# Kernel optimization log

Measured on AMD Instinct MI355X. Metric: run time of the kernel, lower is better.

The kernel has to match this reference:

```python
import jax, jax.numpy as jnp
import numpy as np

C_M = 256
C_Z = 128
S = 256   # number of MSA sequences (global `s` in source)
R = 384   # number of residues (global `r` in source)
C = 32    # per-head channel dim
H = 8     # N_head
EPS = 1e-5


def _layer_norm(x, w, b):
    mu = jnp.mean(x, axis=-1, keepdims=True)
    var = jnp.mean(jnp.square(x - mu), axis=-1, keepdims=True)
    return (x - mu) * jax.lax.rsqrt(var + EPS) * w + b


def setup_inputs() -> dict:
    key = jax.random.key(0)
    ks = jax.random.split(key, 8)
    w = 0.02
    return {
        "msa": jax.random.normal(ks[0], (S, R, C_M), dtype=jnp.float32),
        "pair": jax.random.normal(ks[1], (R, R, C_Z), dtype=jnp.float32),
        "norm_msa_w": jnp.ones((H, C_M), jnp.float32),
        "norm_msa_b": jnp.zeros((H, C_M), jnp.float32),
        "wq": jax.random.normal(ks[2], (H, C, C_M), dtype=jnp.float32) * w,
        "wk": jax.random.normal(ks[3], (H, C, C_M), dtype=jnp.float32) * w,
        "wv": jax.random.normal(ks[4], (H, C, C_M), dtype=jnp.float32) * w,
        "norm_pair_w": jnp.ones((H, C_Z), jnp.float32),
        "norm_pair_b": jnp.zeros((H, C_Z), jnp.float32),
        "wb": jax.random.normal(ks[5], (H, S, C_Z), dtype=jnp.float32) * w,
        "wg": jax.random.normal(ks[6], (H, C, C_M), dtype=jnp.float32) * w,
        "out_w": jax.random.normal(ks[7], (C_M, C * H), dtype=jnp.float32) * w,
        "out_b": jnp.zeros((C_M,), jnp.float32),
    }


def reference(msa, pair, norm_msa_w, norm_msa_b, wq, wk, wv,
              norm_pair_w, norm_pair_b, wb, wg, out_w, out_b):
    inv_sqrt_c = 1.0 / np.sqrt(C).astype(np.float32)
    pair_flat = pair.reshape(-1, C_Z)  # (R*R, C_Z); view(-1, c_z)
    outs = []
    for i in range(H):
        # NOTE: faithful to source — msa is OVERWRITTEN by the per-head norm,
        # so normalization compounds across the head loop.
        msa = _layer_norm(msa, norm_msa_w[i], norm_msa_b[i])
        q = jnp.einsum('src,dc->srd', msa, wq[i])  # (S,R,C)
        k = jnp.einsum('src,dc->srd', msa, wk[i])
        v = jnp.einsum('src,dc->srd', msa, wv[i])
        # pair bias: LN -> Linear(c_z -> s) -> reshape (not transpose!) to (S,R,R)
        b = jnp.einsum('pc,sc->ps', _layer_norm(pair_flat, norm_pair_w[i], norm_pair_b[i]), wb[i])
        b = b.reshape(S, R, R)
        g = jax.nn.sigmoid(jnp.einsum('src,dc->srd', msa, wg[i]))  # (S,R,C)
        logits = inv_sqrt_c * (jnp.einsum('src,stc->srt', q, k) + b)  # (S,R,R)
        a = jax.nn.softmax(logits, axis=-2)  # softmax over QUERY axis, as in source
        o = g * jnp.einsum('srt,stc->src', a, v)  # (S,R,C)
        outs.append(o)
    out = jnp.concatenate(outs, axis=2)  # (S,R,C*H)
    return jnp.einsum('srk,mk->srm', out, out_w) + out_b  # (S,R,C_M)
```

## Files before the change

kernel.cpp:

```cpp
#include <hip/hip_runtime.h>

typedef unsigned short bf16_t;
typedef uint4  __attribute__((may_alias)) uint4_a;
typedef uint2  __attribute__((may_alias)) uint2_a;
typedef float4 __attribute__((may_alias)) float4_a;
typedef short bf16x8 __attribute__((ext_vector_type(8)));
typedef bf16x8 __attribute__((may_alias)) bf16x8_a;
typedef float f32x4 __attribute__((ext_vector_type(4)));

#define MFMA16(a, b, c) __builtin_amdgcn_mfma_f32_16x16x32_bf16((a), (b), (c), 0, 0, 0)

constexpr int kS  = 256;
constexpr int kR  = 384;
constexpr int kCM = 256;
constexpr int kCZ = 128;
constexpr int kC  = 32;
constexpr int kH  = 8;
constexpr int kP  = kR * kR;
constexpr int kM  = kS * kR;

#define EPSF 1e-5f
#define SCALEF 0.17677669529663687f

__device__ __forceinline__ float bf2f(bf16_t u) {
  return __uint_as_float(((unsigned int)u) << 16);
}
__device__ __forceinline__ bf16_t f2bf(float f) {
  unsigned int u = __float_as_uint(f);
  u += 0x7fffu + ((u >> 16) & 1u);
  return (bf16_t)(u >> 16);
}

__global__ __launch_bounds__(256) void k_pair_fused(const float* __restrict__ pair,
                                                    bf16_t* __restrict__ pair_bf,
                                                    float* __restrict__ mu,
                                                    float* __restrict__ rstd) {
  int row = blockIdx.x * 8 + (threadIdx.x >> 5);
  int l = threadIdx.x & 31;
  const float* src = pair + (size_t)row * kCZ + l * 4;
  float4_a x = *(const float4_a*)src;
  float s1 = x.x + x.y + x.z + x.w;
  float s2 = x.x * x.x + x.y * x.y + x.z * x.z + x.w * x.w;
#pragma unroll
  for (int off = 16; off > 0; off >>= 1) {
    s1 += __shfl_xor(s1, off);
    s2 += __shfl_xor(s2, off);
  }
  float m = s1 * (1.0f / kCZ);
  float v = s2 * (1.0f / kCZ) - m * m;
  float rs = rsqrtf(fmaxf(v, 0.0f) + EPSF);
  if (l == 0) {
    mu[row] = m;
    rstd[row] = rs;
  }
  uint2 u;
  u.x = (unsigned)f2bf(x.x) | ((unsigned)f2bf(x.y) << 16);
  u.y = (unsigned)f2bf(x.z) | ((unsigned)f2bf(x.w) << 16);
  *(uint2_a*)(pair_bf + (size_t)row * kCZ + l * 4) = u;
}

__global__ __launch_bounds__(256) void k_msa_ln(const float* __restrict__ src_f,
                                                const bf16_t* __restrict__ src_b,
                                                bf16_t* __restrict__ dst,
                                                const float* __restrict__ wall,
                                                const float* __restrict__ ball,
                                                int head, int first) {
  int row = blockIdx.x * 8 + (threadIdx.x >> 5);
  int l = threadIdx.x & 31;
  int c0 = l * 8;
  float x[8];
  if (first) {
    float4_a a = *(const float4_a*)(src_f + (size_t)row * kCM + c0);
    float4_a b = *(const float4_a*)(src_f + (size_t)row * kCM + c0 + 4);
    x[0] = a.x; x[1] = a.y; x[2] = a.z; x[3] = a.w;
    x[4] = b.x; x[5] = b.y; x[6] = b.z; x[7] = b.w;
  } else {
    union { bf16x8 v; bf16_t h[8]; } uu;
    uu.v = *(const bf16x8_a*)(src_b + (size_t)row * kCM + c0);
#pragma unroll
    for (int j = 0; j < 8; ++j) x[j] = bf2f(uu.h[j]);
  }
  float s1 = 0.f, s2 = 0.f;
#pragma unroll
  for (int j = 0; j < 8; ++j) {
    s1 += x[j];
    s2 += x[j] * x[j];
  }
#pragma unroll
  for (int off = 16; off > 0; off >>= 1) {
    s1 += __shfl_xor(s1, off);
    s2 += __shfl_xor(s2, off);
  }
  float m = s1 * (1.0f / kCM);
  float var = s2 * (1.0f / kCM) - m * m;
  float rs = rsqrtf(fmaxf(var, 0.0f) + EPSF);
  float4_a wa = *(const float4_a*)(wall + head * kCM + c0);
  float4_a wb4 = *(const float4_a*)(wall + head * kCM + c0 + 4);
  float4_a ba = *(const float4_a*)(ball + head * kCM + c0);
  float4_a bb4 = *(const float4_a*)(ball + head * kCM + c0 + 4);
  float wv[8] = {wa.x, wa.y, wa.z, wa.w, wb4.x, wb4.y, wb4.z, wb4.w};
  float bv[8] = {ba.x, ba.y, ba.z, ba.w, bb4.x, bb4.y, bb4.z, bb4.w};
  bf16_t h[8];
#pragma unroll
  for (int j = 0; j < 8; ++j) h[j] = f2bf((x[j] - m) * rs * wv[j] + bv[j]);
  uint4 u;
  u.x = (unsigned)h[0] | ((unsigned)h[1] << 16);
  u.y = (unsigned)h[2] | ((unsigned)h[3] << 16);
  u.z = (unsigned)h[4] | ((unsigned)h[5] << 16);
  u.w = (unsigned)h[6] | ((unsigned)h[7] << 16);
  *(uint4_a*)(dst + (size_t)row * kCM + c0) = u;
}

__global__ __launch_bounds__(256) void k_pack_wcat_all(const float* __restrict__ wq,
                                                       const float* __restrict__ wk,
                                                       const float* __restrict__ wv,
                                                       const float* __restrict__ wg,
                                                       bf16_t* __restrict__ Wcat) {
  int gid = blockIdx.x * 256 + threadIdx.x;
  int head = gid >> 15;
  int idx = gid & 32767;
  int j = idx >> 8;
  int c = idx & 255;
  const float* src = (j < 32) ? wq : (j < 64) ? wk : (j < 96) ? wv : wg;
  int d = j & 31;
  Wcat[gid] = f2bf(src[(head * kC + d) * kCM + c]);
}

__global__ __launch_bounds__(256) void k_pack_bias_all(const float* __restrict__ wb,
                                                       const float* __restrict__ npw,
                                                       const float* __restrict__ npb,
                                                       bf16_t* __restrict__ wbeff,
                                                       float* __restrict__ beta,
                                                       float* __restrict__ sw) {
  int head = blockIdx.x;
  int j = threadIdx.x;
  float sb = 0.f, ssw = 0.f;
  for (int c = 0; c < kCZ; ++c) {
    float w = wb[(head * kS + j) * kCZ + c];
    float e = w * npw[head * kCZ + c] * SCALEF;
    wbeff[(size_t)head * kS * kCZ + j * kCZ + c] = f2bf(e);
    ssw += e;
    sb += w * npb[head * kCZ + c];
  }
  sw[head * kS + j] = ssw;
  beta[head * kS + j] = sb * SCALEF;
}

__global__ __launch_bounds__(256) void k_pack_outw(const float* __restrict__ in,
                                                   bf16_t* __restrict__ out) {
  int i = blockIdx.x * 256 + threadIdx.x;
  out[i] = f2bf(in[i]);
}

__global__ __launch_bounds__(256) void k_gemm_qkvg_mx(const bf16_t* __restrict__ A,
                                                      const bf16_t* __restrict__ B,
                                                      bf16_t* __restrict__ q,
                                                      bf16_t* __restrict__ k,
                                                      bf16_t* __restrict__ v,
                                                      bf16_t* __restrict__ g_all,
                                                      int head) {
  __shared__ bf16_t As[128 * 32];
  __shared__ bf16_t Bs[128 * 32];
  int m0 = blockIdx.x * 128;
  int tid = threadIdx.x;
  int w = tid >> 6, L = tid & 63, l15 = L & 15, q4 = L >> 4;
  int wm = w >> 1, wn = w & 1;
  f32x4 acc[4][4] = {};
  for (int k0 = 0; k0 < 256; k0 += 32) {
#pragma unroll
    for (int rep = 0; rep < 2; ++rep) {
      int idx = tid + rep * 256;
      int row = idx >> 2, sg = idx & 3;
      *(uint4_a*)&As[row * 32 + sg * 8] = *(const uint4_a*)(A + (size_t)(m0 + row) * 256 + k0 + sg * 8);
      *(uint4_a*)&Bs[row * 32 + sg * 8] = *(const uint4_a*)(B + (size_t)row * 256 + k0 + sg * 8);
    }
    __syncthreads();
    bf16x8 af[4], bfr[4];
#pragma unroll
    for (int mt = 0; mt < 4; ++mt) af[mt] = *(const bf16x8_a*)&As[(wm * 64 + mt * 16 + l15) * 32 + q4 * 8];
#pragma unroll
    for (int nt = 0; nt < 4; ++nt) bfr[nt] = *(const bf16x8_a*)&Bs[(wn * 64 + nt * 16 + l15) * 32 + q4 * 8];
#pragma unroll
    for (int mt = 0; mt < 4; ++mt)
#pragma unroll
      for (int nt = 0; nt < 4; ++nt) acc[mt][nt] = MFMA16(af[mt], bfr[nt], acc[mt][nt]);
    __syncthreads();
  }
#pragma unroll
  for (int mt = 0; mt < 4; ++mt)
#pragma unroll
    for (int nt = 0; nt < 4; ++nt) {
      int n = wn * 64 + nt * 16 + l15;
      int mat = n >> 5, d = n & 31;
#pragma unroll
      for (int i = 0; i < 4; ++i) {
        int m = m0 + wm * 64 + mt * 16 + q4 * 4 + i;
        float val = acc[mt][nt][i];
        if (mat == 0) {
          q[(size_t)m * kC + d] = f2bf(val * SCALEF);
        } else if (mat == 1) {
          k[(size_t)m * kC + d] = f2bf(val);
        } else if (mat == 2) {
          v[(size_t)m * kC + d] = f2bf(val);
        } else {
          float sg = 1.0f / (1.0f + __expf(-val));
          g_all[(size_t)m * kCM + head * kC + d] = f2bf(sg);
        }
      }
    }
}

__global__ __launch_bounds__(256) void k_gemm_bias_mx(const bf16_t* __restrict__ A,
                                                      const bf16_t* __restrict__ B,
                                                      const float* __restrict__ mu,
                                                      const float* __restrict__ rstd,
                                                      const float* __restrict__ sw,
                                                      const float* __restrict__ beta,
                                                      bf16_t* __restrict__ Bm) {
  __shared__ bf16_t As[128 * 32];
  __shared__ bf16_t Bs[128 * 32];
  int m0 = blockIdx.x * 128;
  int n0 = blockIdx.y * 128;
  int tid = threadIdx.x;
  int w = tid >> 6, L = tid & 63, l15 = L & 15, q4 = L >> 4;
  int wm = w >> 1, wn = w & 1;
  f32x4 acc[4][4] = {};
  for (int k0 = 0; k0 < 128; k0 += 32) {
#pragma unroll
    for (int rep = 0; rep < 2; ++rep) {
      int idx = tid + rep * 256;
      int row = idx >> 2, sg = idx & 3;
      *(uint4_a*)&As[row * 32 + sg * 8] = *(const uint4_a*)(A + (size_t)(m0 + row) * 128 + k0 + sg * 8);
      *(uint4_a*)&Bs[row * 32 + sg * 8] = *(const uint4_a*)(B + (size_t)(n0 + row) * 128 + k0 + sg * 8);
    }
    __syncthreads();
    bf16x8 af[4], bfr[4];
#pragma unroll
    for (int mt = 0; mt < 4; ++mt) af[mt] = *(const bf16x8_a*)&As[(wm * 64 + mt * 16 + l15) * 32 + q4 * 8];
#pragma unroll
    for (int nt = 0; nt < 4; ++nt) bfr[nt] = *(const bf16x8_a*)&Bs[(wn * 64 + nt * 16 + l15) * 32 + q4 * 8];
#pragma unroll
    for (int mt = 0; mt < 4; ++mt)
#pragma unroll
      for (int nt = 0; nt < 4; ++nt) acc[mt][nt] = MFMA16(af[mt], bfr[nt], acc[mt][nt]);
    __syncthreads();
  }
#pragma unroll
  for (int mt = 0; mt < 4; ++mt)
#pragma unroll
    for (int i = 0; i < 4; ++i) {
      int m = m0 + wm * 64 + mt * 16 + q4 * 4 + i;
      float mp = mu[m], rp = rstd[m];
#pragma unroll
      for (int nt = 0; nt < 4; ++nt) {
        int n = n0 + wn * 64 + nt * 16 + l15;
        float val = rp * (acc[mt][nt][i] - mp * sw[n]) + beta[n];
        Bm[(size_t)m * kS + n] = f2bf(val);
      }
    }
}

__global__ __launch_bounds__(256, 1) void k_attn(const bf16_t* __restrict__ q,
                                                 const bf16_t* __restrict__ kmat,
                                                 const bf16_t* __restrict__ v,
                                                 const bf16_t* __restrict__ Bm,
                                                 float* __restrict__ o0,
                                                 float* __restrict__ o1,
                                                 int head) {
  int tb = blockIdx.x;
  int s  = blockIdx.y;
  int tid = threadIdx.x;
  int w = tid >> 6, L = tid & 63, l15 = L & 15, q4 = L >> 4;
  float* opart = tb ? o1 : o0;
  __shared__ bf16_t vT[32 * 200];
  __shared__ bf16_t Psh[64 * 192];

  int tbase = tb * 192;
#pragma unroll
  for (int rep = 0; rep < 3; ++rep) {
    int idx = tid + rep * 256;
    int t = idx >> 2, sg = idx & 3;
    union { uint4 u; bf16_t h[8]; } uu;
    uu.u = *(const uint4_a*)(v + (size_t)(s * kR + tbase + t) * kC + sg * 8);
#pragma unroll
    for (int j = 0; j < 8; ++j) vT[(sg * 8 + j) * 200 + t] = uu.h[j];
  }
  __syncthreads();
  bf16x8 bfv[12];
#pragma unroll
  for (int kk = 0; kk < 6; ++kk)
#pragma unroll
    for (int ct = 0; ct < 2; ++ct)
      bfv[kk * 2 + ct] = *(const bf16x8_a*)&vT[(ct * 16 + l15) * 200 + kk * 32 + q4 * 8];

  int t0 = tbase + 48 * w;
  const bf16_t* bmS = Bm + (size_t)s * kP;
  f32x4 acc[24][3];
#pragma unroll
  for (int rt = 0; rt < 24; ++rt)
#pragma unroll
    for (int tt = 0; tt < 3; ++tt)
#pragma unroll
      for (int i = 0; i < 4; ++i)
        acc[rt][tt][i] = bf2f(bmS[(size_t)(rt * 16 + q4 * 4 + i) * kR + t0 + tt * 16 + l15]);

  const bf16_t* qs = q + (size_t)s * kR * kC;
  const bf16_t* kp = kmat + (size_t)s * kR * kC;
  bf16x8 bk[3];
#pragma unroll
  for (int tt = 0; tt < 3; ++tt)
    bk[tt] = *(const bf16x8_a*)(kp + (size_t)(t0 + tt * 16 + l15) * kC + q4 * 8);
#pragma unroll
  for (int rt = 0; rt < 24; ++rt) {
    bf16x8 af = *(const bf16x8_a*)(qs + (size_t)(rt * 16 + l15) * kC + q4 * 8);
#pragma unroll
    for (int tt = 0; tt < 3; ++tt) acc[rt][tt] = MFMA16(af, bk[tt], acc[rt][tt]);
  }

  float mx[3] = {-3.0e38f, -3.0e38f, -3.0e38f};
#pragma unroll
  for (int rt = 0; rt < 24; ++rt)
#pragma unroll
    for (int tt = 0; tt < 3; ++tt)
#pragma unroll
      for (int i = 0; i < 4; ++i) mx[tt] = fmaxf(mx[tt], acc[rt][tt][i]);
#pragma unroll
  for (int tt = 0; tt < 3; ++tt) {
    mx[tt] = fmaxf(mx[tt], __shfl_xor(mx[tt], 16));
    mx[tt] = fmaxf(mx[tt], __shfl_xor(mx[tt], 32));
  }
  float sm[3] = {0.f, 0.f, 0.f};
#pragma unroll
  for (int rt = 0; rt < 24; ++rt)
#pragma unroll
    for (int tt = 0; tt < 3; ++tt)
#pragma unroll
      for (int i = 0; i < 4; ++i) {
        float e = __expf(acc[rt][tt][i] - mx[tt]);
        acc[rt][tt][i] = e;
        sm[tt] += e;
      }
#pragma unroll
  for (int tt = 0; tt < 3; ++tt) {
    sm[tt] += __shfl_xor(sm[tt], 16);
    sm[tt] += __shfl_xor(sm[tt], 32);
  }
  float di[3];
#pragma unroll
  for (int tt = 0; tt < 3; ++tt) di[tt] = 1.0f / sm[tt];

#pragma unroll
  for (int c = 0; c < 6; ++c) {
#pragma unroll
    for (int j = 0; j < 4; ++j)
#pragma unroll
      for (int tt = 0; tt < 3; ++tt)
#pragma unroll
        for (int i = 0; i < 4; ++i) {
          int rl = j * 16 + q4 * 4 + i;
          int tl = 48 * w + tt * 16 + l15;
          Psh[rl * 192 + (tl ^ ((rl & 7) << 3))] = f2bf(acc[4 * c + j][tt][i] * di[tt]);
        }
    __syncthreads();
    f32x4 pacc[2] = {};
    int rr = w * 16 + l15;
#pragma unroll
    for (int kk = 0; kk < 6; ++kk) {
      int e = kk * 32 + q4 * 8;
      bf16x8 af = *(const bf16x8_a*)&Psh[rr * 192 + (e ^ ((rr & 7) << 3))];
#pragma unroll
      for (int ct = 0; ct < 2; ++ct) pacc[ct] = MFMA16(af, bfv[kk * 2 + ct], pacc[ct]);
    }
#pragma unroll
    for (int ct = 0; ct < 2; ++ct)
#pragma unroll
      for (int i = 0; i < 4; ++i) {
        int r = c * 64 + w * 16 + q4 * 4 + i;
        int cc = ct * 16 + l15;
        opart[(size_t)(s * kR + r) * kCM + head * kC + cc] = pacc[ct][i];
      }
    __syncthreads();
  }
}

__global__ __launch_bounds__(256) void k_gemm_final_mx(const float* __restrict__ pA,
                                                       const float* __restrict__ pB,
                                                       const bf16_t* __restrict__ gall,
                                                       const bf16_t* __restrict__ Bw,
                                                       const float* __restrict__ bias,
                                                       float* __restrict__ out) {
  __shared__ bf16_t As[2 * 64 * 32];
  __shared__ bf16_t Bs[256 * 32];
  int m0 = blockIdx.x * 64;
  int tid = threadIdx.x;
  int w = tid >> 6, L = tid & 63, l15 = L & 15, q4 = L >> 4;
  f32x4 acc[4][4] = {};
  for (int kc = 0; kc < 256; kc += 32) {
    {
      int row = tid >> 2, sg = tid & 3;
      size_t base = (size_t)(m0 + row) * kCM + kc + sg * 8;
      float4_a a0 = *(const float4_a*)(pA + base);
      float4_a a1 = *(const float4_a*)(pA + base + 4);
      float4_a b0 = *(const float4_a*)(pB + base);
      float4_a b1 = *(const float4_a*)(pB + base + 4);
      union { bf16x8 v; bf16_t h[8]; } gg;
      gg.v = *(const bf16x8_a*)(gall + base);
      float ff[8] = {a0.x + b0.x, a0.y + b0.y, a0.z + b0.z, a0.w + b0.w,
                     a1.x + b1.x, a1.y + b1.y, a1.z + b1.z, a1.w + b1.w};
#pragma unroll
      for (int j = 0; j < 8; ++j) ff[j] *= bf2f(gg.h[j]);
      uint4 uh, ul;
      bf16_t hi[8], lo[8];
#pragma unroll
      for (int j = 0; j < 8; ++j) {
        hi[j] = f2bf(ff[j]);
        lo[j] = f2bf(ff[j] - bf2f(hi[j]));
      }
      uh.x = (unsigned)hi[0] | ((unsigned)hi[1] << 16); uh.y = (unsigned)hi[2] | ((unsigned)hi[3] << 16);
      uh.z = (unsigned)hi[4] | ((unsigned)hi[5] << 16); uh.w = (unsigned)hi[6] | ((unsigned)hi[7] << 16);
      ul.x = (unsigned)lo[0] | ((unsigned)lo[1] << 16); ul.y = (unsigned)lo[2] | ((unsigned)lo[3] << 16);
      ul.z = (unsigned)lo[4] | ((unsigned)lo[5] << 16); ul.w = (unsigned)lo[6] | ((unsigned)lo[7] << 16);
      *(uint4_a*)&As[row * 32 + sg * 8] = uh;
      *(uint4_a*)&As[2048 + row * 32 + sg * 8] = ul;
    }
#pragma unroll
    for (int rep = 0; rep < 4; ++rep) {
      int idx = tid + rep * 256;
      int row = idx >> 2, sg = idx & 3;
      *(uint4_a*)&Bs[row * 32 + sg * 8] = *(const uint4_a*)(Bw + (size_t)row * kCM + kc + sg * 8);
    }
    __syncthreads();
    bf16x8 bfr[4];
#pragma unroll
    for (int nt = 0; nt < 4; ++nt) bfr[nt] = *(const bf16x8_a*)&Bs[(w * 64 + nt * 16 + l15) * 32 + q4 * 8];
#pragma unroll
    for (int half = 0; half < 2; ++half)
#pragma unroll
      for (int mt = 0; mt < 4; ++mt) {
        bf16x8 af = *(const bf16x8_a*)&As[half * 2048 + (mt * 16 + l15) * 32 + q4 * 8];
#pragma unroll
        for (int nt = 0; nt < 4; ++nt) acc[mt][nt] = MFMA16(af, bfr[nt], acc[mt][nt]);
      }
    __syncthreads();
  }
#pragma unroll
  for (int mt = 0; mt < 4; ++mt)
#pragma unroll
    for (int nt = 0; nt < 4; ++nt) {
      int n = w * 64 + nt * 16 + l15;
      float bn = bias[n];
#pragma unroll
      for (int i = 0; i < 4; ++i) {
        int m = m0 + mt * 16 + q4 * 4 + i;
        out[(size_t)m * kCM + n] = acc[mt][nt][i] + bn;
      }
    }
}

extern "C" void kernel_launch(void* const* d_in, const int* in_sizes, int n_in,
                              void* d_out, int out_size, void* d_ws, size_t ws_size,
                              hipStream_t stream) {
  (void)in_sizes; (void)n_in; (void)out_size; (void)ws_size;
  const float* msa_in = (const float*)d_in[0];
  const float* pair   = (const float*)d_in[1];
  const float* nmw    = (const float*)d_in[2];
  const float* nmb    = (const float*)d_in[3];
  const float* wq     = (const float*)d_in[4];
  const float* wk     = (const float*)d_in[5];
  const float* wv     = (const float*)d_in[6];
  const float* npw    = (const float*)d_in[7];
  const float* npb    = (const float*)d_in[8];
  const float* wb     = (const float*)d_in[9];
  const float* wg     = (const float*)d_in[10];
  const float* outw   = (const float*)d_in[11];
  const float* outb   = (const float*)d_in[12];
  float* out = (float*)d_out;

  char* ws = (char*)d_ws;
  size_t off = 0;
  bf16_t* msa_cur  = (bf16_t*)(ws + off); off += (size_t)kM * kCM * 2;
  bf16_t* pair_bf  = (bf16_t*)(ws + off); off += (size_t)kP * kCZ * 2;
  bf16_t* Bm       = (bf16_t*)(ws + off); off += (size_t)kP * kS * 2;
  bf16_t* qb       = (bf16_t*)(ws + off); off += (size_t)kM * kC * 2;
  bf16_t* kb       = (bf16_t*)(ws + off); off += (size_t)kM * kC * 2;
  bf16_t* vb       = (bf16_t*)(ws + off); off += (size_t)kM * kC * 2;
  bf16_t* g_all    = (bf16_t*)(ws + off); off += (size_t)kM * kCM * 2;
  float*  pB       = (float*)(ws + off);  off += (size_t)kM * kCM * 4;
  float* mu_p      = (float*)(ws + off);  off += (size_t)kP * 4;
  float* rstd_p    = (float*)(ws + off);  off += (size_t)kP * 4;
  bf16_t* Wcat_all = (bf16_t*)(ws + off); off += (size_t)kH * 128 * 256 * 2;
  bf16_t* wbef_all = (bf16_t*)(ws + off); off += (size_t)kH * 256 * 128 * 2;
  bf16_t* outw_bf  = (bf16_t*)(ws + off); off += (size_t)256 * 256 * 2;
  float* beta_all  = (float*)(ws + off);  off += (size_t)kH * 256 * 4;
  float* sw_all    = (float*)(ws + off);  off += (size_t)kH * 256 * 4;

  k_pair_fused<<<kP / 8, 256, 0, stream>>>(pair, pair_bf, mu_p, rstd_p);
  k_pack_outw<<<256, 256, 0, stream>>>(outw, outw_bf);
  k_pack_wcat_all<<<kH * 128, 256, 0, stream>>>(wq, wk, wv, wg, Wcat_all);
  k_pack_bias_all<<<kH, 256, 0, stream>>>(wb, npw, npb, wbef_all, beta_all, sw_all);

  for (int h = 0; h < kH; ++h) {
    k_msa_ln<<<kM / 8, 256, 0, stream>>>(msa_in, msa_cur, msa_cur, nmw, nmb, h, h == 0 ? 1 : 0);
    k_gemm_qkvg_mx<<<kM / 128, 256, 0, stream>>>(msa_cur, Wcat_all + (size_t)h * 128 * 256,
                                                 qb, kb, vb, g_all, h);
    k_gemm_bias_mx<<<dim3(kP / 128, 2), 256, 0, stream>>>(pair_bf, wbef_all + (size_t)h * 256 * 128,
                                                          mu_p, rstd_p,
                                                          sw_all + h * 256, beta_all + h * 256, Bm);
    k_attn<<<dim3(2, kS), 256, 0, stream>>>(qb, kb, vb, Bm, out, pB, h);
  }

  k_gemm_final_mx<<<kM / 64, 256, 0, stream>>>(out, pB, g_all, outw_bf, outb, out);
}
```

Baseline: 1.325 ms.

## Fuse pair-bias GEMM into attention kernel and emit gated bf16 hi/lo output

Removes the separate pair-bias GEMM that wrote a large bf16 bias tensor (R*R*S) to global memory each head. Each attention block now computes its sequence's bias slice on the fly from pair_bf and the bias weights into LDS, then loads it into the logits accumulators. The two key-halves are handled in one block, which drops the split fp32 partial outputs. Gating and the hi/lo bf16 split move into the attention epilogue, so the final GEMM just loads bf16. The trade-off is half as many blocks (256), heavy LDS use and more serialized work per block. That could reduce occupancy and overlap.

```diff
diff --git a/kernel.cpp b/kernel.cpp
--- a/kernel.cpp
+++ b/kernel.cpp
@@ -21,6 +21,7 @@
 
 #define EPSF 1e-5f
 #define SCALEF 0.17677669529663687f
+#define BSWZ(i) ((i) ^ ((((i) >> 8) & 7) << 4))
 
 __device__ __forceinline__ float bf2f(bf16_t u) {
   return __uint_as_float(((unsigned int)u) << 16);
@@ -210,182 +211,224 @@
     }
 }
 
-__global__ __launch_bounds__(256) void k_gemm_bias_mx(const bf16_t* __restrict__ A,
-                                                      const bf16_t* __restrict__ B,
-                                                      const float* __restrict__ mu,
-                                                      const float* __restrict__ rstd,
-                                                      const float* __restrict__ sw,
-                                                      const float* __restrict__ beta,
-                                                      bf16_t* __restrict__ Bm) {
-  __shared__ bf16_t As[128 * 32];
-  __shared__ bf16_t Bs[128 * 32];
-  int m0 = blockIdx.x * 128;
-  int n0 = blockIdx.y * 128;
+__global__ __launch_bounds__(256, 1) void k_attn_fused(const bf16_t* __restrict__ q,
+                                                       const bf16_t* __restrict__ kmat,
+                                                       const bf16_t* __restrict__ v,
+                                                       const bf16_t* __restrict__ pair_bf,
+                                                       const bf16_t* __restrict__ wbeff,
+                                                       const float* __restrict__ mu,
+                                                       const float* __restrict__ rstd,
+                                                       const float* __restrict__ sw,
+                                                       const float* __restrict__ beta,
+                                                       const bf16_t* __restrict__ g_all,
+                                                       bf16_t* __restrict__ ohi,
+                                                       bf16_t* __restrict__ olo,
+                                                       int head) {
+  int s = blockIdx.x;
   int tid = threadIdx.x;
   int w = tid >> 6, L = tid & 63, l15 = L & 15, q4 = L >> 4;
-  int wm = w >> 1, wn = w & 1;
-  f32x4 acc[4][4] = {};
-  for (int k0 = 0; k0 < 128; k0 += 32) {
-#pragma unroll
-    for (int rep = 0; rep < 2; ++rep) {
-      int idx = tid + rep * 256;
-      int row = idx >> 2, sg = idx & 3;
-      *(uint4_a*)&As[row * 32 + sg * 8] = *(const uint4_a*)(A + (size_t)(m0 + row) * 128 + k0 + sg * 8);
-      *(uint4_a*)&Bs[row * 32 + sg * 8] = *(const uint4_a*)(B + (size_t)(n0 + row) * 128 + k0 + sg * 8);
-    }
-    __syncthreads();
-    bf16x8 af[4], bfr[4];
-#pragma unroll
-    for (int mt = 0; mt < 4; ++mt) af[mt] = *(const bf16x8_a*)&As[(wm * 64 + mt * 16 + l15) * 32 + q4 * 8];
-#pragma unroll
-    for (int nt = 0; nt < 4; ++nt) bfr[nt] = *(const bf16x8_a*)&Bs[(wn * 64 + nt * 16 + l15) * 32 + q4 * 8];
-#pragma unroll
-    for (int mt = 0; mt < 4; ++mt)
-#pragma unroll
-      for (int nt = 0; nt < 4; ++nt) acc[mt][nt] = MFMA16(af[mt], bfr[nt], acc[mt][nt]);
-    __syncthreads();
-  }
-#pragma unroll
-  for (int mt = 0; mt < 4; ++mt)
-#pragma unroll
-    for (int i = 0; i < 4; ++i) {
-      int m = m0 + wm * 64 + mt * 16 + q4 * 4 + i;
-      float mp = mu[m], rp = rstd[m];
-#pragma unroll
-      for (int nt = 0; nt < 4; ++nt) {
-        int n = n0 + wn * 64 + nt * 16 + l15;
-        float val = rp * (acc[mt][nt][i] - mp * sw[n]) + beta[n];
-        Bm[(size_t)m * kS + n] = f2bf(val);
-      }
-    }
-}
-
-__global__ __launch_bounds__(256, 1) void k_attn(const bf16_t* __restrict__ q,
-                                                 const bf16_t* __restrict__ kmat,
-                                                 const bf16_t* __restrict__ v,
-                                                 const bf16_t* __restrict__ Bm,
-                                                 float* __restrict__ o0,
-                                                 float* __restrict__ o1,
-                                                 int head) {
-  int tb = blockIdx.x;
-  int s  = blockIdx.y;
-  int tid = threadIdx.x;
-  int w = tid >> 6, L = tid & 63, l15 = L & 15, q4 = L >> 4;
-  float* opart = tb ? o1 : o0;
+  __shared__ bf16_t Wb[256 * 128];
+  __shared__ bf16_t Ap[48 * 128];
+  __shared__ bf16_t BiasL[12288];
   __shared__ bf16_t vT[32 * 200];
   __shared__ bf16_t Psh[64 * 192];
 
-  int tbase = tb * 192;
-#pragma unroll
-  for (int rep = 0; rep < 3; ++rep) {
+  int xw = (l15 & 7) << 3;
+
+#pragma unroll
+  for (int rep = 0; rep < 16; ++rep) {
     int idx = tid + rep * 256;
-    int t = idx >> 2, sg = idx & 3;
-    union { uint4 u; bf16_t h[8]; } uu;
-    uu.u = *(const uint4_a*)(v + (size_t)(s * kR + tbase + t) * kC + sg * 8);
-#pragma unroll
-    for (int j = 0; j < 8; ++j) vT[(sg * 8 + j) * 200 + t] = uu.h[j];
+    int row = idx >> 4, kg = idx & 15;
+    *(uint4_a*)&Wb[row * 128 + ((kg * 8) ^ ((row & 7) << 3))] =
+        *(const uint4_a*)(wbeff + (size_t)row * 128 + kg * 8);
+  }
+  float swv[4], betav[4];
+#pragma unroll
+  for (int nt = 0; nt < 4; ++nt) {
+    int n = w * 64 + nt * 16 + l15;
+    swv[nt] = sw[n];
+    betav[nt] = beta[n];
   }
   __syncthreads();
-  bf16x8 bfv[12];
-#pragma unroll
-  for (int kk = 0; kk < 6; ++kk)
-#pragma unroll
-    for (int ct = 0; ct < 2; ++ct)
-      bfv[kk * 2 + ct] = *(const bf16x8_a*)&vT[(ct * 16 + l15) * 200 + kk * 32 + q4 * 8];
-
-  int t0 = tbase + 48 * w;
-  const bf16_t* bmS = Bm + (size_t)s * kP;
-  f32x4 acc[24][3];
-#pragma unroll
-  for (int rt = 0; rt < 24; ++rt)
-#pragma unroll
-    for (int tt = 0; tt < 3; ++tt)
-#pragma unroll
-      for (int i = 0; i < 4; ++i)
-        acc[rt][tt][i] = bf2f(bmS[(size_t)(rt * 16 + q4 * 4 + i) * kR + t0 + tt * 16 + l15]);
 
   const bf16_t* qs = q + (size_t)s * kR * kC;
   const bf16_t* kp = kmat + (size_t)s * kR * kC;
-  bf16x8 bk[3];
-#pragma unroll
-  for (int tt = 0; tt < 3; ++tt)
-    bk[tt] = *(const bf16x8_a*)(kp + (size_t)(t0 + tt * 16 + l15) * kC + q4 * 8);
-#pragma unroll
-  for (int rt = 0; rt < 24; ++rt) {
-    bf16x8 af = *(const bf16x8_a*)(qs + (size_t)(rt * 16 + l15) * kC + q4 * 8);
-#pragma unroll
-    for (int tt = 0; tt < 3; ++tt) acc[rt][tt] = MFMA16(af, bk[tt], acc[rt][tt]);
-  }
-
-  float mx[3] = {-3.0e38f, -3.0e38f, -3.0e38f};
-#pragma unroll
-  for (int rt = 0; rt < 24; ++rt)
+  int prow = tid >> 4, pkg = tid & 15;
+  const bf16_t* pbase = pair_bf + ((size_t)s * 576) * 128;
+
+  f32x4 opacc[6][2] = {};
+
+  for (int tb = 0; tb < 2; ++tb) {
+    int tbase = tb * 192;
+    int t0 = tbase + 48 * w;
+    f32x4 acc[24][3];
+
+    uint4 pf0, pf1, pf2;
+    pf0 = *(const uint4_a*)(pbase + (size_t)(prow)*128 + pkg * 8);
+    pf1 = *(const uint4_a*)(pbase + (size_t)(16 + prow) * 128 + pkg * 8);
+    pf2 = *(const uint4_a*)(pbase + (size_t)(32 + prow) * 128 + pkg * 8);
+#pragma unroll
+    for (int rc = 0; rc < 12; ++rc) {
+      *(uint4_a*)&Ap[prow * 128 + ((pkg * 8) ^ ((prow & 7) << 3))] = pf0;
+      *(uint4_a*)&Ap[(16 + prow) * 128 + ((pkg * 8) ^ ((prow & 7) << 3))] = pf1;
+      *(uint4_a*)&Ap[(32 + prow) * 128 + ((pkg * 8) ^ ((prow & 7) << 3))] = pf2;
+      if (rc < 11) {
+        const bf16_t* nb = pbase + (size_t)(rc + 1) * 48 * 128;
+        pf0 = *(const uint4_a*)(nb + (size_t)(prow)*128 + pkg * 8);
+        pf1 = *(const uint4_a*)(nb + (size_t)(16 + prow) * 128 + pkg * 8);
+        pf2 = *(const uint4_a*)(nb + (size_t)(32 + prow) * 128 + pkg * 8);
+      }
+      __syncthreads();
+      f32x4 acc2[3][4] = {};
+#pragma unroll
+      for (int k0 = 0; k0 < 128; k0 += 32) {
+        bf16x8 af[3], bfr[4];
+#pragma unroll
+        for (int mt = 0; mt < 3; ++mt)
+          af[mt] = *(const bf16x8_a*)&Ap[(mt * 16 + l15) * 128 + ((k0 + q4 * 8) ^ xw)];
+#pragma unroll
+        for (int nt = 0; nt < 4; ++nt) {
+          int n = w * 64 + nt * 16 + l15;
+          bfr[nt] = *(const bf16x8_a*)&Wb[n * 128 + ((k0 + q4 * 8) ^ xw)];
+        }
+#pragma unroll
+        for (int mt = 0; mt < 3; ++mt)
+#pragma unroll
+          for (int nt = 0; nt < 4; ++nt) acc2[mt][nt] = MFMA16(af[mt], bfr[nt], acc2[mt][nt]);
+      }
+      int pg = s * 576 + rc * 48;
+#pragma unroll
+      for (int mt = 0; mt < 3; ++mt)
+#pragma unroll
+        for (int i = 0; i < 4; ++i) {
+          int m_loc = mt * 16 + q4 * 4 + i;
+          float mp = mu[pg + m_loc], rp = rstd[pg + m_loc];
+#pragma unroll
+          for (int nt = 0; nt < 4; ++nt) {
+            int n = w * 64 + nt * 16 + l15;
+            int fl = m_loc * 256 + n;
+            BiasL[BSWZ(fl)] = f2bf(rp * (acc2[mt][nt][i] - mp * swv[nt]) + betav[nt]);
+          }
+        }
+      __syncthreads();
+#pragma unroll
+      for (int rt2 = 0; rt2 < 2; ++rt2)
+#pragma unroll
+        for (int tt = 0; tt < 3; ++tt)
+#pragma unroll
+          for (int i = 0; i < 4; ++i) {
+            int r_loc = rt2 * 16 + q4 * 4 + i;
+            int t = t0 + tt * 16 + l15;
+            int fl = r_loc * 384 + t;
+            acc[rc * 2 + rt2][tt][i] = bf2f(BiasL[BSWZ(fl)]);
+          }
+    }
+
+    bf16x8 bk[3];
 #pragma unroll
     for (int tt = 0; tt < 3; ++tt)
-#pragma unroll
-      for (int i = 0; i < 4; ++i) mx[tt] = fmaxf(mx[tt], acc[rt][tt][i]);
-#pragma unroll
-  for (int tt = 0; tt < 3; ++tt) {
-    mx[tt] = fmaxf(mx[tt], __shfl_xor(mx[tt], 16));
-    mx[tt] = fmaxf(mx[tt], __shfl_xor(mx[tt], 32));
-  }
-  float sm[3] = {0.f, 0.f, 0.f};
-#pragma unroll
-  for (int rt = 0; rt < 24; ++rt)
-#pragma unroll
-    for (int tt = 0; tt < 3; ++tt)
-#pragma unroll
-      for (int i = 0; i < 4; ++i) {
-        float e = __expf(acc[rt][tt][i] - mx[tt]);
-        acc[rt][tt][i] = e;
-        sm[tt] += e;
-      }
-#pragma unroll
-  for (int tt = 0; tt < 3; ++tt) {
-    sm[tt] += __shfl_xor(sm[tt], 16);
-    sm[tt] += __shfl_xor(sm[tt], 32);
-  }
-  float di[3];
-#pragma unroll
-  for (int tt = 0; tt < 3; ++tt) di[tt] = 1.0f / sm[tt];
-
-#pragma unroll
-  for (int c = 0; c < 6; ++c) {
-#pragma unroll
-    for (int j = 0; j < 4; ++j)
+      bk[tt] = *(const bf16x8_a*)(kp + (size_t)(t0 + tt * 16 + l15) * kC + q4 * 8);
+#pragma unroll
+    for (int rt = 0; rt < 24; ++rt) {
+      bf16x8 af = *(const bf16x8_a*)(qs + (size_t)(rt * 16 + l15) * kC + q4 * 8);
+#pragma unroll
+      for (int tt = 0; tt < 3; ++tt) acc[rt][tt] = MFMA16(af, bk[tt], acc[rt][tt]);
+    }
+
+    float mx[3] = {-3.0e38f, -3.0e38f, -3.0e38f};
+#pragma unroll
+    for (int rt = 0; rt < 24; ++rt)
 #pragma unroll
       for (int tt = 0; tt < 3; ++tt)
 #pragma unroll
+        for (int i = 0; i < 4; ++i) mx[tt] = fmaxf(mx[tt], acc[rt][tt][i]);
+#pragma unroll
+    for (int tt = 0; tt < 3; ++tt) {
+      mx[tt] = fmaxf(mx[tt], __shfl_xor(mx[tt], 16));
+      mx[tt] = fmaxf(mx[tt], __shfl_xor(mx[tt], 32));
+    }
+    float sm[3] = {0.f, 0.f, 0.f};
+#pragma unroll
+    for (int rt = 0; rt < 24; ++rt)
+#pragma unroll
+      for (int tt = 0; tt < 3; ++tt)
+#pragma unroll
         for (int i = 0; i < 4; ++i) {
-          int rl = j * 16 + q4 * 4 + i;
-          int tl = 48 * w + tt * 16 + l15;
-          Psh[rl * 192 + (tl ^ ((rl & 7) << 3))] = f2bf(acc[4 * c + j][tt][i] * di[tt]);
+          float e = __expf(acc[rt][tt][i] - mx[tt]);
+          acc[rt][tt][i] = e;
+          sm[tt] += e;
         }
+#pragma unroll
+    for (int tt = 0; tt < 3; ++tt) {
+      sm[tt] += __shfl_xor(sm[tt], 16);
+      sm[tt] += __shfl_xor(sm[tt], 32);
+    }
+    float di[3];
+#pragma unroll
+    for (int tt = 0; tt < 3; ++tt) di[tt] = 1.0f / sm[tt];
+
+#pragma unroll
+    for (int rep = 0; rep < 3; ++rep) {
+      int idx = tid + rep * 256;
+      int t = idx >> 2, sg = idx & 3;
+      union { uint4 u; bf16_t h[8]; } uu;
+      uu.u = *(const uint4_a*)(v + (size_t)(s * kR + tbase + t) * kC + sg * 8);
+#pragma unroll
+      for (int j = 0; j < 8; ++j) vT[(sg * 8 + j) * 200 + t] = uu.h[j];
+    }
     __syncthreads();
-    f32x4 pacc[2] = {};
-    int rr = w * 16 + l15;
-#pragma unroll
-    for (int kk = 0; kk < 6; ++kk) {
-      int e = kk * 32 + q4 * 8;
-      bf16x8 af = *(const bf16x8_a*)&Psh[rr * 192 + (e ^ ((rr & 7) << 3))];
-#pragma unroll
-      for (int ct = 0; ct < 2; ++ct) pacc[ct] = MFMA16(af, bfv[kk * 2 + ct], pacc[ct]);
-    }
+    bf16x8 bfv[12];
+#pragma unroll
+    for (int kk = 0; kk < 6; ++kk)
+#pragma unroll
+      for (int ct = 0; ct < 2; ++ct)
+        bfv[kk * 2 + ct] = *(const bf16x8_a*)&vT[(ct * 16 + l15) * 200 + kk * 32 + q4 * 8];
+
+#pragma unroll
+    for (int c = 0; c < 6; ++c) {
+#pragma unroll
+      for (int j = 0; j < 4; ++j)
+#pragma unroll
+        for (int tt = 0; tt < 3; ++tt)
+#pragma unroll
+          for (int i = 0; i < 4; ++i) {
+            int rl = j * 16 + q4 * 4 + i;
+            int tl = 48 * w + tt * 16 + l15;
+            Psh[rl * 192 + (tl ^ ((rl & 7) << 3))] = f2bf(acc[4 * c + j][tt][i] * di[tt]);
+          }
+      __syncthreads();
+      int rr = w * 16 + l15;
+#pragma unroll
+      for (int kk = 0; kk < 6; ++kk) {
+        int e = kk * 32 + q4 * 8;
+        bf16x8 af = *(const bf16x8_a*)&Psh[rr * 192 + (e ^ ((rr & 7) << 3))];
+#pragma unroll
+        for (int ct = 0; ct < 2; ++ct) opacc[c][ct] = MFMA16(af, bfv[kk * 2 + ct], opacc[c][ct]);
+      }
+      __syncthreads();
+    }
+  }
+
+  const bf16_t* gp = g_all + (size_t)s * kR * kCM + head * kC;
+#pragma unroll
+  for (int c = 0; c < 6; ++c)
 #pragma unroll
     for (int ct = 0; ct < 2; ++ct)
 #pragma unroll
       for (int i = 0; i < 4; ++i) {
         int r = c * 64 + w * 16 + q4 * 4 + i;
         int cc = ct * 16 + l15;
-        opart[(size_t)(s * kR + r) * kCM + head * kC + cc] = pacc[ct][i];
-      }
-    __syncthreads();
-  }
-}
-
-__global__ __launch_bounds__(256) void k_gemm_final_mx(const float* __restrict__ pA,
-                                                       const float* __restrict__ pB,
-                                                       const bf16_t* __restrict__ gall,
+        float val = opacc[c][ct][i] * bf2f(gp[(size_t)r * kCM + cc]);
+        bf16_t hi = f2bf(val);
+        bf16_t lo = f2bf(val - bf2f(hi));
+        size_t oidx = (size_t)(s * kR + r) * kCM + head * kC + cc;
+        ohi[oidx] = hi;
+        olo[oidx] = lo;
+      }
+}
+
+__global__ __launch_bounds__(256) void k_gemm_final_mx(const bf16_t* __restrict__ Ahi,
+                                                       const bf16_t* __restrict__ Alo,
                                                        const bf16_t* __restrict__ Bw,
                                                        const float* __restrict__ bias,
                                                        float* __restrict__ out) {
@@ -399,29 +442,8 @@
     {
       int row = tid >> 2, sg = tid & 3;
       size_t base = (size_t)(m0 + row) * kCM + kc + sg * 8;
-      float4_a a0 = *(const float4_a*)(pA + base);
-      float4_a a1 = *(const float4_a*)(pA + base + 4);
-      float4_a b0 = *(const float4_a*)(pB + base);
-      float4_a b1 = *(const float4_a*)(pB + base + 4);
-      union { bf16x8 v; bf16_t h[8]; } gg;
-      gg.v = *(const bf16x8_a*)(gall + base);
-      float ff[8] = {a0.x + b0.x, a0.y + b0.y, a0.z + b0.z, a0.w + b0.w,
-                     a1.x + b1.x, a1.y + b1.y, a1.z + b1.z, a1.w + b1.w};
-#pragma unroll
-      for (int j = 0; j < 8; ++j) ff[j] *= bf2f(gg.h[j]);
-      uint4 uh, ul;
-      bf16_t hi[8], lo[8];
-#pragma unroll
-      for (int j = 0; j < 8; ++j) {
-        hi[j] = f2bf(ff[j]);
-        lo[j] = f2bf(ff[j] - bf2f(hi[j]));
-      }
-      uh.x = (unsigned)hi[0] | ((unsigned)hi[1] << 16); uh.y = (unsigned)hi[2] | ((unsigned)hi[3] << 16);
-      uh.z = (unsigned)hi[4] | ((unsigned)hi[5] << 16); uh.w = (unsigned)hi[6] | ((unsigned)hi[7] << 16);
-      ul.x = (unsigned)lo[0] | ((unsigned)lo[1] << 16); ul.y = (unsigned)lo[2] | ((unsigned)lo[3] << 16);
-      ul.z = (unsigned)lo[4] | ((unsigned)lo[5] << 16); ul.w = (unsigned)lo[6] | ((unsigned)lo[7] << 16);
-      *(uint4_a*)&As[row * 32 + sg * 8] = uh;
-      *(uint4_a*)&As[2048 + row * 32 + sg * 8] = ul;
+      *(uint4_a*)&As[row * 32 + sg * 8] = *(const uint4_a*)(Ahi + base);
+      *(uint4_a*)&As[2048 + row * 32 + sg * 8] = *(const uint4_a*)(Alo + base);
     }
 #pragma unroll
     for (int rep = 0; rep < 4; ++rep) {
@@ -480,12 +502,12 @@
   size_t off = 0;
   bf16_t* msa_cur  = (bf16_t*)(ws + off); off += (size_t)kM * kCM * 2;
   bf16_t* pair_bf  = (bf16_t*)(ws + off); off += (size_t)kP * kCZ * 2;
-  bf16_t* Bm       = (bf16_t*)(ws + off); off += (size_t)kP * kS * 2;
   bf16_t* qb       = (bf16_t*)(ws + off); off += (size_t)kM * kC * 2;
   bf16_t* kb       = (bf16_t*)(ws + off); off += (size_t)kM * kC * 2;
   bf16_t* vb       = (bf16_t*)(ws + off); off += (size_t)kM * kC * 2;
   bf16_t* g_all    = (bf16_t*)(ws + off); off += (size_t)kM * kCM * 2;
-  float*  pB       = (float*)(ws + off);  off += (size_t)kM * kCM * 4;
+  bf16_t* ohi      = (bf16_t*)(ws + off); off += (size_t)kM * kCM * 2;
+  bf16_t* olo      = (bf16_t*)(ws + off); off += (size_t)kM * kCM * 2;
   float* mu_p      = (float*)(ws + off);  off += (size_t)kP * 4;
   float* rstd_p    = (float*)(ws + off);  off += (size_t)kP * 4;
   bf16_t* Wcat_all = (bf16_t*)(ws + off); off += (size_t)kH * 128 * 256 * 2;
@@ -503,11 +525,12 @@
     k_msa_ln<<<kM / 8, 256, 0, stream>>>(msa_in, msa_cur, msa_cur, nmw, nmb, h, h == 0 ? 1 : 0);
     k_gemm_qkvg_mx<<<kM / 128, 256, 0, stream>>>(msa_cur, Wcat_all + (size_t)h * 128 * 256,
                                                  qb, kb, vb, g_all, h);
-    k_gemm_bias_mx<<<dim3(kP / 128, 2), 256, 0, stream>>>(pair_bf, wbef_all + (size_t)h * 256 * 128,
-                                                          mu_p, rstd_p,
-                                                          sw_all + h * 256, beta_all + h * 256, Bm);
-    k_attn<<<dim3(2, kS), 256, 0, stream>>>(qb, kb, vb, Bm, out, pB, h);
-  }
-
-  k_gemm_final_mx<<<kM / 64, 256, 0, stream>>>(out, pB, g_all, outw_bf, outb, out);
-}
+    k_attn_fused<<<kS, 256, 0, stream>>>(qb, kb, vb, pair_bf,
+                                         wbef_all + (size_t)h * 256 * 128,
+                                         mu_p, rstd_p,
+                                         sw_all + h * 256, beta_all + h * 256,
+                                         g_all, ohi, olo, h);
+  }
+
+  k_gemm_final_mx<<<kM / 64, 256, 0, stream>>>(ohi, olo, outw_bf, outb, out);
+}
```

New measurement: 3.725 ms. 181% more time.
